# Performance work log

Hardware: AMD Instinct MI355X
Metric: run time of the kernel (lower is better)

The kernel has to match this reference:

```python
import jax, jax.numpy as jnp
import numpy as np

KS = 3      # kernel size
PAD = 1     # zero padding
STRIDE = 1
N = KS * KS # 9 sampling points per pixel


def _deform_conv(feature, offset, weight):
    """DeformConv2d: bilinear sample at learned offsets then 3x3 conv (no bias)."""
    b, c, h, w = feature.shape
    x = jnp.pad(feature, ((0, 0), (0, 0), (PAD, PAD), (PAD, PAD)))
    hp, wp = h + 2 * PAD, w + 2 * PAD
    dt = feature.dtype
    # p_n: kernel grid offsets, x(rows) first then y(cols) -> (2N,)
    rng = jnp.arange(-(KS - 1) // 2, (KS - 1) // 2 + 1, dtype=dt)
    pn_x, pn_y = jnp.meshgrid(rng, rng, indexing='ij')
    # p_0: base sampling grid starting at 1 (accounts for zero padding)
    p0_x, p0_y = jnp.meshgrid(jnp.arange(1, h + 1, dtype=dt),
                              jnp.arange(1, w + 1, dtype=dt), indexing='ij')
    # sampling locations p = p_0 + p_n + offset, split into x/y -> (b,h,w,N)
    off = jnp.transpose(offset, (0, 2, 3, 1))  # (b,h,w,2N)
    px = p0_x[None, :, :, None] + pn_x.reshape(-1)[None, None, None, :] + off[..., :N]
    py = p0_y[None, :, :, None] + pn_y.reshape(-1)[None, None, None, :] + off[..., N:]
    q_lt_x = jnp.clip(jnp.floor(px), 0, hp - 1)
    q_lt_y = jnp.clip(jnp.floor(py), 0, wp - 1)
    q_rb_x = jnp.clip(jnp.floor(px) + 1, 0, hp - 1)
    q_rb_y = jnp.clip(jnp.floor(py) + 1, 0, wp - 1)
    px = jnp.clip(px, 0, hp - 1)
    py = jnp.clip(py, 0, wp - 1)
    # bilinear weights for the 4 corners
    g_lt = (1 + (q_lt_x - px)) * (1 + (q_lt_y - py))
    g_rb = (1 - (q_rb_x - px)) * (1 - (q_rb_y - py))
    g_lb = (1 + (q_lt_x - px)) * (1 - (q_rb_y - py))
    g_rt = (1 - (q_rb_x - px)) * (1 + (q_lt_y - py))
    x_flat = x.reshape(b, c, hp * wp)

    def gather(qx, qy):
        idx = (qx * wp + qy).astype(jnp.int32).reshape(b, 1, -1)
        v = jnp.take_along_axis(x_flat, jnp.broadcast_to(idx, (b, c, h * w * N)), axis=2)
        return v.reshape(b, c, h, w, N)

    x_off = (g_lt[:, None] * gather(q_lt_x, q_lt_y)
             + g_rb[:, None] * gather(q_rb_x, q_rb_y)
             + g_lb[:, None] * gather(q_lt_x, q_rb_y)
             + g_rt[:, None] * gather(q_rb_x, q_lt_y))  # (b,c,h,w,N)
    # equivalent of _reshape_x_offset + conv(ks, stride=ks)
    x_off = x_off.reshape(b, c, h, w, KS, KS)
    return jnp.einsum('bchwij,ocij->bohw', x_off, weight)


def setup_inputs() -> dict:
    key = jax.random.key(0)
    k1, k2, k3 = jax.random.split(key, 3)
    B, C, H, W = 4, 256, 64, 64
    feature = jax.random.normal(k1, (B, C, H, W), dtype=jnp.float32)
    offset = jax.random.normal(k2, (B, 2 * N, H, W), dtype=jnp.float32)
    weight = jax.random.normal(k3, (C, C, KS, KS), dtype=jnp.float32) / np.sqrt(C * N)
    return {"feature": feature, "offset": offset, "weight": weight}


def reference(feature, offset, weight):
    f1 = jax.nn.relu(_deform_conv(feature, offset, weight))
    return jax.nn.relu(f1 + feature)
```

## Files before the change

### kernel.cpp

```cpp
#include <hip/hip_runtime.h>

#define HW    4096
#define J_TOT 16384
#define K_TOT 2304
#define C_CH  256

typedef unsigned short u16;
typedef unsigned int   u32;
typedef __attribute__((ext_vector_type(8))) short short8;
typedef __attribute__((ext_vector_type(4))) float f32x4;
typedef __attribute__((ext_vector_type(8))) unsigned short us8;

__device__ __forceinline__ float b2f(u16 u) { return __uint_as_float(((u32)u) << 16); }
__device__ __forceinline__ u16 f2b(float x) {
  u32 u = __float_as_uint(x);
  u += 0x7FFFu + ((u >> 16) & 1u);
  return (u16)(u >> 16);
}

__device__ __forceinline__ void gload_lds16(const u16* g, u16* l) {
  __builtin_amdgcn_global_load_lds(
      (__attribute__((address_space(1))) void*)(void*)g,
      (__attribute__((address_space(3))) void*)(void*)l, 16, 0, 0);
}

__global__ void k_detect(const u16* __restrict__ f, int* __restrict__ flag) {
  __shared__ int sh[256];
  int t = threadIdx.x;
  int hits = 0;
  for (int i = t; i < 2048; i += 256) {
    u16 u = f[2 * i];
    int e = (u >> 7) & 0xFF;
    hits += (e >= 100 && e <= 141) ? 1 : 0;
  }
  sh[t] = hits;
  __syncthreads();
  if (t == 0) {
    int s = 0;
    for (int i = 0; i < 256; i++) s += sh[i];
    flag[0] = (s > 1024) ? 1 : 0;
  }
}

__global__ void k_transpose(const void* __restrict__ featv, u16* __restrict__ ftr,
                            const int* __restrict__ flag) {
  __shared__ u16 tile[32][33];
  int isbf = *flag;
  int b = blockIdx.z;
  int hw0 = blockIdx.x << 5;
  int c0 = blockIdx.y << 5;
  int tx = threadIdx.x;
  int ty = threadIdx.y;
  if (isbf) {
    const u16* f = (const u16*)featv;
#pragma unroll
    for (int i = 0; i < 4; i++) {
      int c = c0 + ty + i * 8;
      tile[ty + i * 8][tx] = f[(((size_t)(b * C_CH + c)) << 12) + hw0 + tx];
    }
  } else {
    const float* f = (const float*)featv;
#pragma unroll
    for (int i = 0; i < 4; i++) {
      int c = c0 + ty + i * 8;
      tile[ty + i * 8][tx] = f2b(f[(((size_t)(b * C_CH + c)) << 12) + hw0 + tx]);
    }
  }
  __syncthreads();
#pragma unroll
  for (int i = 0; i < 4; i++) {
    int hw = hw0 + ty + i * 8;
    ftr[(((size_t)(b * HW + hw)) << 8) + c0 + tx] = tile[tx][ty + i * 8];
  }
}

__global__ void k_wconv(const void* __restrict__ wv, u16* __restrict__ Wr,
                        const int* __restrict__ flag) {
  int isbf = *flag;
  int idx = blockIdx.x * 256 + threadIdx.x;
  if (idx >= C_CH * K_TOT) return;
  int c = idx & 255;
  int n = (idx >> 8) % 9;
  int o = idx / K_TOT;
  int src = (o * 256 + c) * 9 + n;
  if (isbf) Wr[idx] = ((const u16*)wv)[src];
  else      Wr[idx] = f2b(((const float*)wv)[src]);
}

#define NT 36

#define A_DMA(bufi)                                                          \
  do {                                                                       \
    gload_lds16(asrc0, &As[bufi][wave * 2048]);                              \
    gload_lds16(asrc1, &As[bufi][wave * 2048 + 512]);                        \
    gload_lds16(asrc2, &As[bufi][wave * 2048 + 1024]);                       \
    gload_lds16(asrc3, &As[bufi][wave * 2048 + 1536]);                       \
    asrc0 += 64; asrc1 += 64; asrc2 += 64; asrc3 += 64;                      \
  } while (0)

#define PLOAD(tile)                                                          \
  do {                                                                       \
    int np = (tile) >> 2, c0 = ((tile) & 3) << 6;                            \
    w0 = gs[np][0][pp]; w1 = gs[np][1][pp];                                  \
    w2 = gs[np][2][pp]; w3 = gs[np][3][pp];                                  \
    q0 = *(const us8*)(ftr + isx[np][0][pp] + c0 + cb8);                     \
    q1 = *(const us8*)(ftr + isx[np][1][pp] + c0 + cb8);                     \
    q2 = *(const us8*)(ftr + isx[np][2][pp] + c0 + cb8);                     \
    q3 = *(const us8*)(ftr + isx[np][3][pp] + c0 + cb8);                     \
  } while (0)

#define PFIN(bufi)                                                           \
  do {                                                                       \
    us8 ov;                                                                  \
    _Pragma("unroll")                                                        \
    for (int i = 0; i < 8; i++) {                                            \
      float v = w0 * b2f(q0[i]) + w1 * b2f(q1[i]) +                          \
                w2 * b2f(q2[i]) + w3 * b2f(q3[i]);                           \
      ov[i] = f2b(v);                                                        \
    }                                                                        \
    *(us8*)(&Bs[bufi][bofs]) = ov;                                           \
  } while (0)

#define GEMM_COMPUTE(bufi)                                                   \
  do {                                                                       \
    short8 af[2][2], bf[4][2];                                               \
    _Pragma("unroll")                                                        \
    for (int kk = 0; kk < 2; kk++) {                                         \
      int go = (((kk << 2) + lk) ^ swz) << 3;                                \
      _Pragma("unroll")                                                      \
      for (int oi = 0; oi < 2; oi++)                                         \
        af[oi][kk] = *(const short8*)(As[bufi] + (wave * 32 + oi * 16 + lr) * 64 + go); \
      _Pragma("unroll")                                                      \
      for (int ji = 0; ji < 4; ji++)                                         \
        bf[ji][kk] = *(const short8*)(Bs[bufi] + (ji * 16 + lr) * 64 + go);  \
    }                                                                        \
    __builtin_amdgcn_s_setprio(1);                                           \
    _Pragma("unroll")                                                        \
    for (int kk = 0; kk < 2; kk++)                                           \
      _Pragma("unroll")                                                      \
      for (int oi = 0; oi < 2; oi++)                                         \
        _Pragma("unroll")                                                    \
        for (int ji = 0; ji < 4; ji++)                                       \
          acc[oi][ji] = __builtin_amdgcn_mfma_f32_16x16x32_bf16(             \
              af[oi][kk], bf[ji][kk], acc[oi][ji], 0, 0, 0);                 \
    __builtin_amdgcn_s_setprio(0);                                           \
  } while (0)

__global__ __launch_bounds__(512) void k_gemm(const u16* __restrict__ Wr,
                                              const u16* __restrict__ ftr,
                                              const void* __restrict__ offv,
                                              const void* __restrict__ featv,
                                              void* __restrict__ outv,
                                              const int* __restrict__ flag) {
  __shared__ u16 As[2][256 * 64];
  __shared__ u16 Bs[2][64 * 64];
  __shared__ float gs[9][4][64];
  __shared__ int   isx[9][4][64];
  int isbf = *flag;
  int j0 = blockIdx.x << 6;
  int b = j0 >> 12;
  int hw0 = j0 & (HW - 1);
  int t = threadIdx.x;
  int wave = t >> 6, lane = t & 63;
  int lr = lane & 15, lk = lane >> 4;
  int swz = lr & 7;

  for (int e = t; e < 576; e += 512) {
    int n = e >> 6, p = e & 63;
    int hw = hw0 + p;
    int h = hw >> 6, w = hw & 63;
    size_t obi = (((size_t)(b * 18 + n)) << 12) + hw;
    float ox, oy;
    if (isbf) {
      const u16* po = (const u16*)offv;
      ox = b2f(po[obi]);
      oy = b2f(po[obi + (9u << 12)]);
    } else {
      const float* po = (const float*)offv;
      ox = po[obi];
      oy = po[obi + (9u << 12)];
    }
    int ki = n / 3, kj = n % 3;
    float px = (float)(h + ki) + ox;
    float py = (float)(w + kj) + oy;
    float fx = floorf(px), fy = floorf(py);
    float qltx = fminf(fmaxf(fx, 0.f), 65.f);
    float qlty = fminf(fmaxf(fy, 0.f), 65.f);
    float qrbx = fminf(fmaxf(fx + 1.f, 0.f), 65.f);
    float qrby = fminf(fmaxf(fy + 1.f, 0.f), 65.f);
    float pcx = fminf(fmaxf(px, 0.f), 65.f);
    float pcy = fminf(fmaxf(py, 0.f), 65.f);
    float dltx = 1.f + (qltx - pcx);
    float drbx = 1.f - (qrbx - pcx);
    float dlty = 1.f + (qlty - pcy);
    float drby = 1.f - (qrby - pcy);
    float g0 = dltx * dlty;
    float g1 = drbx * drby;
    float g2 = dltx * drby;
    float g3 = drbx * dlty;
    int x0 = (int)qltx, y0 = (int)qlty, x1 = (int)qrbx, y1 = (int)qrby;
    int v0 = (x0 >= 1 && x0 <= 64 && y0 >= 1 && y0 <= 64);
    int v1 = (x1 >= 1 && x1 <= 64 && y1 >= 1 && y1 <= 64);
    int v2 = (x0 >= 1 && x0 <= 64 && y1 >= 1 && y1 <= 64);
    int v3 = (x1 >= 1 && x1 <= 64 && y0 >= 1 && y0 <= 64);
    int base = b << 12;
    isx[n][0][p] = v0 ? ((base + ((x0 - 1) << 6) + (y0 - 1)) << 8) : 0;
    isx[n][1][p] = v1 ? ((base + ((x1 - 1) << 6) + (y1 - 1)) << 8) : 0;
    isx[n][2][p] = v2 ? ((base + ((x0 - 1) << 6) + (y1 - 1)) << 8) : 0;
    isx[n][3][p] = v3 ? ((base + ((x1 - 1) << 6) + (y0 - 1)) << 8) : 0;
    gs[n][0][p] = v0 ? g0 : 0.f;
    gs[n][1][p] = v1 ? g1 : 0.f;
    gs[n][2][p] = v2 ? g2 : 0.f;
    gs[n][3][p] = v3 ? g3 : 0.f;
  }

  f32x4 acc[2][4];
  f32x4 zero = {0.f, 0.f, 0.f, 0.f};
#pragma unroll
  for (int i = 0; i < 2; i++)
#pragma unroll
    for (int j = 0; j < 4; j++) acc[i][j] = zero;

  int rb = lane >> 3;
  int cs = ((lane & 7) ^ rb) << 3;
  const u16* asrc0 = Wr + (size_t)(wave * 32 +  0 + rb) * K_TOT + cs;
  const u16* asrc1 = Wr + (size_t)(wave * 32 +  8 + rb) * K_TOT + cs;
  const u16* asrc2 = Wr + (size_t)(wave * 32 + 16 + rb) * K_TOT + cs;
  const u16* asrc3 = Wr + (size_t)(wave * 32 + 24 + rb) * K_TOT + cs;

  int pp = t >> 3, cg = t & 7;
  int bofs = pp * 64 + ((cg ^ (pp & 7)) << 3);
  int cb8 = cg << 3;

  __syncthreads();

  us8 q0, q1, q2, q3;
  float w0, w1, w2, w3;

  PLOAD(0);
  A_DMA(0);
  PFIN(0);
  __syncthreads();

  for (int tt = 0; tt < NT - 1; ++tt) {
    int cbuf = tt & 1, nbuf = cbuf ^ 1;
    PLOAD(tt + 1);
    A_DMA(nbuf);
    GEMM_COMPUTE(cbuf);
    PFIN(nbuf);
    __syncthreads();
  }
  GEMM_COMPUTE((NT - 1) & 1);

  int lq = lane >> 4;
#pragma unroll
  for (int oi = 0; oi < 2; oi++) {
#pragma unroll
    for (int ji = 0; ji < 4; ji++) {
      int j = j0 + ji * 16 + lr;
      int bb_ = j >> 12, hw = j & (HW - 1);
      int o0 = wave * 32 + oi * 16 + lq * 4;
#pragma unroll
      for (int r = 0; r < 4; r++) {
        size_t oidx = (((size_t)(bb_ * C_CH + o0 + r)) << 12) + hw;
        float v = acc[oi][ji][r];
        v = fmaxf(v, 0.f);
        float ft = isbf ? b2f(((const u16*)featv)[oidx]) : ((const float*)featv)[oidx];
        v = fmaxf(v + ft, 0.f);
        if (isbf) ((u16*)outv)[oidx] = f2b(v);
        else      ((float*)outv)[oidx] = v;
      }
    }
  }
}

extern "C" void kernel_launch(void* const* d_in, const int* in_sizes, int n_in,
                              void* d_out, int out_size, void* d_ws, size_t ws_size,
                              hipStream_t stream) {
  const void* feat = d_in[0];
  const void* offs = d_in[1];
  const void* wght = d_in[2];

  const size_t off_flag = 0;
  const size_t off_wr   = 256;
  const size_t off_ftr  = off_wr + (size_t)1179648;
  const size_t need     = off_ftr + (size_t)8388608;
  if (ws_size < need) return;

  char* ws = (char*)d_ws;
  int* flag = (int*)(ws + off_flag);
  u16* Wr   = (u16*)(ws + off_wr);
  u16* ftr  = (u16*)(ws + off_ftr);

  k_detect<<<1, 256, 0, stream>>>((const u16*)feat, flag);
  k_transpose<<<dim3(128, 8, 4), dim3(32, 8), 0, stream>>>(feat, ftr, flag);
  k_wconv<<<K_TOT, 256, 0, stream>>>(wght, Wr, flag);
  k_gemm<<<J_TOT / 64, 512, 0, stream>>>(Wr, ftr, offs, feat, d_out, flag);
}
```

Baseline: 140.8 us.

## Split GEMM output channels across two blocks and fuse prep kernels

The main GEMM grid is doubled by splitting the 256 output channels into two 128-channel halves per block. Each wave now computes a 32x32 tile instead of 32x64, which halves the A-tile LDS footprint and raises the block count for better CU occupancy. The cost is that the bilinear gather and offset computation for the B operand is repeated in both halves. The transpose and weight-conversion kernels are also merged into one launch to save a kernel launch.

```diff
diff --git a/kernel.cpp b/kernel.cpp
--- a/kernel.cpp
+++ b/kernel.cpp
@@ -42,60 +42,60 @@
   }
 }
 
-__global__ void k_transpose(const void* __restrict__ featv, u16* __restrict__ ftr,
-                            const int* __restrict__ flag) {
-  __shared__ u16 tile[32][33];
+__global__ void k_prep(const void* __restrict__ featv, u16* __restrict__ ftr,
+                       const void* __restrict__ wv, u16* __restrict__ Wr,
+                       const int* __restrict__ flag) {
   int isbf = *flag;
-  int b = blockIdx.z;
-  int hw0 = blockIdx.x << 5;
-  int c0 = blockIdx.y << 5;
   int tx = threadIdx.x;
   int ty = threadIdx.y;
-  if (isbf) {
-    const u16* f = (const u16*)featv;
+  int z = blockIdx.z;
+  if (z < 4) {
+    __shared__ u16 tile[32][33];
+    int b = z;
+    int hw0 = blockIdx.x << 5;
+    int c0 = blockIdx.y << 5;
+    if (isbf) {
+      const u16* f = (const u16*)featv;
+#pragma unroll
+      for (int i = 0; i < 4; i++) {
+        int c = c0 + ty + i * 8;
+        tile[ty + i * 8][tx] = f[(((size_t)(b * C_CH + c)) << 12) + hw0 + tx];
+      }
+    } else {
+      const float* f = (const float*)featv;
+#pragma unroll
+      for (int i = 0; i < 4; i++) {
+        int c = c0 + ty + i * 8;
+        tile[ty + i * 8][tx] = f2b(f[(((size_t)(b * C_CH + c)) << 12) + hw0 + tx]);
+      }
+    }
+    __syncthreads();
 #pragma unroll
     for (int i = 0; i < 4; i++) {
-      int c = c0 + ty + i * 8;
-      tile[ty + i * 8][tx] = f[(((size_t)(b * C_CH + c)) << 12) + hw0 + tx];
+      int hw = hw0 + ty + i * 8;
+      ftr[(((size_t)(b * HW + hw)) << 8) + c0 + tx] = tile[tx][ty + i * 8];
     }
   } else {
-    const float* f = (const float*)featv;
-#pragma unroll
-    for (int i = 0; i < 4; i++) {
-      int c = c0 + ty + i * 8;
-      tile[ty + i * 8][tx] = f2b(f[(((size_t)(b * C_CH + c)) << 12) + hw0 + tx]);
-    }
-  }
-  __syncthreads();
-#pragma unroll
-  for (int i = 0; i < 4; i++) {
-    int hw = hw0 + ty + i * 8;
-    ftr[(((size_t)(b * HW + hw)) << 8) + c0 + tx] = tile[tx][ty + i * 8];
-  }
-}
-
-__global__ void k_wconv(const void* __restrict__ wv, u16* __restrict__ Wr,
-                        const int* __restrict__ flag) {
-  int isbf = *flag;
-  int idx = blockIdx.x * 256 + threadIdx.x;
-  if (idx >= C_CH * K_TOT) return;
-  int c = idx & 255;
-  int n = (idx >> 8) % 9;
-  int o = idx / K_TOT;
-  int src = (o * 256 + c) * 9 + n;
-  if (isbf) Wr[idx] = ((const u16*)wv)[src];
-  else      Wr[idx] = f2b(((const float*)wv)[src]);
+    int bid = blockIdx.x + (blockIdx.y << 7);
+    int flat = ty * 32 + tx;
+    for (int idx = bid * 256 + flat; idx < C_CH * K_TOT; idx += 1024 * 256) {
+      int c = idx & 255;
+      int n = (idx >> 8) % 9;
+      int o = idx / K_TOT;
+      int src = (o * 256 + c) * 9 + n;
+      if (isbf) Wr[idx] = ((const u16*)wv)[src];
+      else      Wr[idx] = f2b(((const float*)wv)[src]);
+    }
+  }
 }
 
 #define NT 36
 
 #define A_DMA(bufi)                                                          \
   do {                                                                       \
-    gload_lds16(asrc0, &As[bufi][wave * 2048]);                              \
-    gload_lds16(asrc1, &As[bufi][wave * 2048 + 512]);                        \
-    gload_lds16(asrc2, &As[bufi][wave * 2048 + 1024]);                       \
-    gload_lds16(asrc3, &As[bufi][wave * 2048 + 1536]);                       \
-    asrc0 += 64; asrc1 += 64; asrc2 += 64; asrc3 += 64;                      \
+    gload_lds16(asrc0, &As[bufi][wave * 1024]);                              \
+    gload_lds16(asrc1, &As[bufi][wave * 1024 + 512]);                        \
+    asrc0 += 64; asrc1 += 64;                                                \
   } while (0)
 
 #define PLOAD(tile)                                                          \
@@ -123,16 +123,16 @@
 
 #define GEMM_COMPUTE(bufi)                                                   \
   do {                                                                       \
-    short8 af[2][2], bf[4][2];                                               \
+    short8 af[2][2], bf[2][2];                                               \
     _Pragma("unroll")                                                        \
     for (int kk = 0; kk < 2; kk++) {                                         \
       int go = (((kk << 2) + lk) ^ swz) << 3;                                \
       _Pragma("unroll")                                                      \
       for (int oi = 0; oi < 2; oi++)                                         \
-        af[oi][kk] = *(const short8*)(As[bufi] + (wave * 32 + oi * 16 + lr) * 64 + go); \
+        af[oi][kk] = *(const short8*)(As[bufi] + (wo * 32 + oi * 16 + lr) * 64 + go); \
       _Pragma("unroll")                                                      \
-      for (int ji = 0; ji < 4; ji++)                                         \
-        bf[ji][kk] = *(const short8*)(Bs[bufi] + (ji * 16 + lr) * 64 + go);  \
+      for (int ji = 0; ji < 2; ji++)                                         \
+        bf[ji][kk] = *(const short8*)(Bs[bufi] + (wj * 32 + ji * 16 + lr) * 64 + go); \
     }                                                                        \
     __builtin_amdgcn_s_setprio(1);                                           \
     _Pragma("unroll")                                                        \
@@ -140,7 +140,7 @@
       _Pragma("unroll")                                                      \
       for (int oi = 0; oi < 2; oi++)                                         \
         _Pragma("unroll")                                                    \
-        for (int ji = 0; ji < 4; ji++)                                       \
+        for (int ji = 0; ji < 2; ji++)                                       \
           acc[oi][ji] = __builtin_amdgcn_mfma_f32_16x16x32_bf16(             \
               af[oi][kk], bf[ji][kk], acc[oi][ji], 0, 0, 0);                 \
     __builtin_amdgcn_s_setprio(0);                                           \
@@ -152,16 +152,18 @@
                                               const void* __restrict__ featv,
                                               void* __restrict__ outv,
                                               const int* __restrict__ flag) {
-  __shared__ u16 As[2][256 * 64];
+  __shared__ u16 As[2][128 * 64];
   __shared__ u16 Bs[2][64 * 64];
   __shared__ float gs[9][4][64];
   __shared__ int   isx[9][4][64];
   int isbf = *flag;
   int j0 = blockIdx.x << 6;
+  int ob0 = blockIdx.y << 7;
   int b = j0 >> 12;
   int hw0 = j0 & (HW - 1);
   int t = threadIdx.x;
   int wave = t >> 6, lane = t & 63;
+  int wj = wave >> 2, wo = wave & 3;
   int lr = lane & 15, lk = lane >> 4;
   int swz = lr & 7;
 
@@ -214,19 +216,17 @@
     gs[n][3][p] = v3 ? g3 : 0.f;
   }
 
-  f32x4 acc[2][4];
+  f32x4 acc[2][2];
   f32x4 zero = {0.f, 0.f, 0.f, 0.f};
 #pragma unroll
   for (int i = 0; i < 2; i++)
 #pragma unroll
-    for (int j = 0; j < 4; j++) acc[i][j] = zero;
+    for (int j = 0; j < 2; j++) acc[i][j] = zero;
 
   int rb = lane >> 3;
   int cs = ((lane & 7) ^ rb) << 3;
-  const u16* asrc0 = Wr + (size_t)(wave * 32 +  0 + rb) * K_TOT + cs;
-  const u16* asrc1 = Wr + (size_t)(wave * 32 +  8 + rb) * K_TOT + cs;
-  const u16* asrc2 = Wr + (size_t)(wave * 32 + 16 + rb) * K_TOT + cs;
-  const u16* asrc3 = Wr + (size_t)(wave * 32 + 24 + rb) * K_TOT + cs;
+  const u16* asrc0 = Wr + (size_t)(ob0 + wave * 16 + 0 + rb) * K_TOT + cs;
+  const u16* asrc1 = Wr + (size_t)(ob0 + wave * 16 + 8 + rb) * K_TOT + cs;
 
   int pp = t >> 3, cg = t & 7;
   int bofs = pp * 64 + ((cg ^ (pp & 7)) << 3);
@@ -256,10 +256,10 @@
 #pragma unroll
   for (int oi = 0; oi < 2; oi++) {
 #pragma unroll
-    for (int ji = 0; ji < 4; ji++) {
-      int j = j0 + ji * 16 + lr;
+    for (int ji = 0; ji < 2; ji++) {
+      int j = j0 + wj * 32 + ji * 16 + lr;
       int bb_ = j >> 12, hw = j & (HW - 1);
-      int o0 = wave * 32 + oi * 16 + lq * 4;
+      int o0 = ob0 + wo * 32 + oi * 16 + lq * 4;
 #pragma unroll
       for (int r = 0; r < 4; r++) {
         size_t oidx = (((size_t)(bb_ * C_CH + o0 + r)) << 12) + hw;
@@ -293,7 +293,6 @@
   u16* ftr  = (u16*)(ws + off_ftr);
 
   k_detect<<<1, 256, 0, stream>>>((const u16*)feat, flag);
-  k_transpose<<<dim3(128, 8, 4), dim3(32, 8), 0, stream>>>(feat, ftr, flag);
-  k_wconv<<<K_TOT, 256, 0, stream>>>(wght, Wr, flag);
-  k_gemm<<<J_TOT / 64, 512, 0, stream>>>(Wr, ftr, offs, feat, d_out, flag);
-}
+  k_prep<<<dim3(128, 8, 5), dim3(32, 8), 0, stream>>>(feat, ftr, wght, Wr, flag);
+  k_gemm<<<dim3(J_TOT / 64, 2), 512, 0, stream>>>(Wr, ftr, offs, feat, d_out, flag);
+}
```

Result: faster. 136.4 us (-3.1%).
